# Optimization experiments

Measured on AMD Instinct MI355X. Metric: run time of the kernel, lower is better.

## Reference

```python
import jax, jax.numpy as jnp
import numpy as np

EPS = 1e-5


def conv2d(x, w, b, groups=1):
    # x: NCHW, w: OIHW, stride 1, SAME padding (== padding=k//2 for odd k)
    y = jax.lax.conv_general_dilated(
        x, w, window_strides=(1, 1), padding='SAME',
        dimension_numbers=('NCHW', 'OIHW', 'NCHW'),
        feature_group_count=groups)
    return y + b[None, :, None, None]


def gelu(x):
    return jax.nn.gelu(x, approximate=False)  # torch default GELU is exact erf


def adaptive_feature_norm(x, gamma, beta, s1w, s1b, s2w, s2b):
    # stats_net: GAP -> 1x1 conv -> ReLU -> 1x1 conv -> chunk into (gamma_a, beta_a)
    pooled = x.mean(axis=(2, 3), keepdims=True)                 # [B,C,1,1]
    h = jax.nn.relu(conv2d(pooled, s1w, s1b))
    stats = conv2d(h, s2w, s2b)                                 # [B,2C,1,1]
    ag, ab = jnp.split(stats, 2, axis=1)
    mean = x.mean(axis=(2, 3), keepdims=True)
    n = x.shape[2] * x.shape[3]
    var = ((x - mean) ** 2).sum(axis=(2, 3), keepdims=True) / (n - 1)  # unbiased, torch.var_mean default
    x_norm = (x - mean) * jax.lax.rsqrt(var + EPS)
    return (1 + ag) * gamma * x_norm + ab * beta


def setup_inputs() -> dict:
    key = jax.random.key(0)
    ks = jax.random.split(key, 40)
    B, C, H, W = 16, 256, 96, 96
    c4 = C // 4

    def n(k, shape, s=0.02):
        return jax.random.normal(k, shape, dtype=jnp.float32) * s

    inp = dict(
        x=jax.random.normal(ks[0], (B, C, H, W), dtype=jnp.float32),
        # branch1 conv1: dim -> dim//4, 3x3
        b1_conv1_w=n(ks[1], (c4, C, 3, 3)), b1_conv1_b=jnp.zeros((c4,), jnp.float32),
        # AFN on dim//4
        afn1_gamma=jnp.ones((1, c4, 1, 1), jnp.float32), afn1_beta=jnp.zeros((1, c4, 1, 1), jnp.float32),
        afn1_s1_w=n(ks[2], (c4 // 4, c4, 1, 1)), afn1_s1_b=jnp.zeros((c4 // 4,), jnp.float32),
        afn1_s2_w=n(ks[3], (c4 * 2, c4 // 4, 1, 1)), afn1_s2_b=jnp.zeros((c4 * 2,), jnp.float32),
        # branch1 conv2: dim//4 -> dim, 3x3
        b1_conv2_w=n(ks[4], (C, c4, 3, 3)), b1_conv2_b=jnp.zeros((C,), jnp.float32),
        # AFN on dim
        afn2_gamma=jnp.ones((1, C, 1, 1), jnp.float32), afn2_beta=jnp.zeros((1, C, 1, 1), jnp.float32),
        afn2_s1_w=n(ks[5], (c4, C, 1, 1)), afn2_s1_b=jnp.zeros((c4,), jnp.float32),
        afn2_s2_w=n(ks[6], (C * 2, c4, 1, 1)), afn2_s2_b=jnp.zeros((C * 2,), jnp.float32),
        # attention qkv/proj (1x1 convs)
        qkv_w=n(ks[7], (3 * C, C, 1, 1)), qkv_b=jnp.zeros((3 * C,), jnp.float32),
        proj_w=n(ks[8], (C, C, 1, 1)), proj_b=jnp.zeros((C,), jnp.float32),
        # 3 frequency decomposition branches, stacked
        # grouped 3x3 conv: groups=C//4, in=C (4 per group), out=C//4 (1 per group) -> weight [C//4, 4, 3, 3]
        fd_dw_w=n(ks[9], (3, c4, 4, 3, 3)), fd_dw_b=jnp.zeros((3, c4), jnp.float32),
        fd_pw_w=n(ks[10], (3, C, c4, 1, 1)), fd_pw_b=jnp.zeros((3, C), jnp.float32),
        freq_weights=jnp.ones((3,), jnp.float32),
        # router: GAP -> 1x1 conv -> softmax over 2 routes
        router_w=n(ks[11], (2, C, 1, 1)), router_b=jnp.zeros((2,), jnp.float32),
    )
    return inp


def reference(x,
              b1_conv1_w, b1_conv1_b, afn1_gamma, afn1_beta, afn1_s1_w, afn1_s1_b, afn1_s2_w, afn1_s2_b,
              b1_conv2_w, b1_conv2_b, afn2_gamma, afn2_beta, afn2_s1_w, afn2_s1_b, afn2_s2_w, afn2_s2_b,
              qkv_w, qkv_b, proj_w, proj_b, fd_dw_w, fd_dw_b, fd_pw_w, fd_pw_b, freq_weights,
              router_w, router_b):
    B, C, H, W = x.shape
    num_heads = 8
    hd = C // num_heads
    scale = C ** (-0.5)

    # ---- router ----
    pooled = x.mean(axis=(2, 3), keepdims=True)
    route = jax.nn.softmax(conv2d(pooled, router_w, router_b), axis=1)  # [B,2,1,1]

    # ---- branch1: conv -> AFN -> GELU -> conv -> AFN ----
    h = conv2d(x, b1_conv1_w, b1_conv1_b)
    h = adaptive_feature_norm(h, afn1_gamma, afn1_beta, afn1_s1_w, afn1_s1_b, afn1_s2_w, afn1_s2_b)
    h = gelu(h)
    h = conv2d(h, b1_conv2_w, b1_conv2_b)
    out1 = adaptive_feature_norm(h, afn2_gamma, afn2_beta, afn2_s1_w, afn2_s1_b, afn2_s2_w, afn2_s2_b)

    # ---- branch2: multi-scale frequency attention ----
    qkv = conv2d(x, qkv_w, qkv_b).reshape(B, 3, num_heads, hd, H, W)
    q, k, v = qkv[:, 0], qkv[:, 1], qkv[:, 2]          # [B, nh, hd, H, W]
    # attn over spatial rows: q @ k^T contracts W -> [B, nh, hd, H, H]
    attn = jnp.einsum('bndhw,bndgw->bndhg', q, k) * scale
    attn = jax.nn.softmax(attn, axis=-1)
    a = jnp.einsum('bndhg,bndgw->bndhw', attn, v)       # [B, nh, hd, H, W]
    # torch: .transpose(1, 2).reshape(B, C, H, W)  (hd-major channel order)
    a = a.transpose(0, 2, 1, 3, 4).reshape(B, C, H, W)
    x_attn = conv2d(a, proj_w, proj_b)

    fw = jax.nn.softmax(freq_weights, axis=0)
    freq_out = 0.0
    for i in range(3):
        f = conv2d(x, fd_dw_w[i], fd_dw_b[i], groups=C // 4)
        f = conv2d(gelu(f), fd_pw_w[i], fd_pw_b[i])
        freq_out = freq_out + fw[i] * f
    out2 = x_attn + freq_out

    return x + route[:, 0:1, :, :] * out1 + route[:, 1:2, :, :] * out2
```

## Files before the change

### kernel.cpp

```cpp
#include <hip/hip_runtime.h>
#include <hip/hip_bf16.h>
#include <math.h>
#include <stdint.h>

#define BB 16
#define CC 256
#define C4 64
#define HH 96
#define WW 96
#define HW 9216
#define EPSF 1e-5f

using bf16x8 = __attribute__((ext_vector_type(8))) short;
using bf16x4 = __attribute__((ext_vector_type(4))) short;
using f32x4  = __attribute__((ext_vector_type(4))) float;

#define GLD16(g, l) \
    __builtin_amdgcn_global_load_lds((const __attribute__((address_space(1))) unsigned int*)(g), \
                                     (__attribute__((address_space(3))) unsigned int*)(l), 16, 0, 0)

__device__ inline float bf2f_bits(short s) {
    return __uint_as_float(((unsigned int)(unsigned short)s) << 16);
}
__device__ inline short f2bf_bits(float f) {
    unsigned int u = __float_as_uint(f);
    return (short)((u + 0x7fffu + ((u >> 16) & 1u)) >> 16);
}

__global__ void zero_n_kernel(unsigned int* __restrict__ p, int n) {
    int i = blockIdx.x * 256 + threadIdx.x;
    if (i < n) p[i] = 0u;
}

__global__ void router_kernel(const float* __restrict__ pooled, const float* __restrict__ rw,
                              const float* __restrict__ rb, const float* __restrict__ fwts,
                              float* __restrict__ route, float* __restrict__ fw) {
    int t = threadIdx.x;
    const float invhw = 1.f / (float)HW;
    if (t < BB) {
        float l0 = rb[0], l1 = rb[1];
        for (int c = 0; c < CC; ++c) {
            float p = pooled[t * CC + c] * invhw;
            l0 += p * rw[c];
            l1 += p * rw[CC + c];
        }
        float m = fmaxf(l0, l1);
        float e0 = __expf(l0 - m), e1 = __expf(l1 - m);
        float inv = 1.f / (e0 + e1);
        route[t * 2 + 0] = e0 * inv;
        route[t * 2 + 1] = e1 * inv;
    }
    if (t == BB) {
        float a = fwts[0], b = fwts[1], c = fwts[2];
        float m = fmaxf(a, fmaxf(b, c));
        float e0 = __expf(a - m), e1 = __expf(b - m), e2 = __expf(c - m);
        float inv = 1.f / (e0 + e1 + e2);
        fw[0] = e0 * inv; fw[1] = e1 * inv; fw[2] = e2 * inv;
    }
}

__global__ void pack_w3x3_kernel(const float* __restrict__ w, __hip_bfloat16* __restrict__ wt,
                                 int COUT, int CINW) {
    int idx = blockIdx.x * 256 + threadIdx.x;
    int total = COUT * 9 * CINW;
    if (idx >= total) return;
    int ci = idx % CINW; int rest = idx / CINW; int tau = rest % 9; int co = rest / 9;
    wt[idx] = __float2bfloat16(w[((size_t)co * CINW + ci) * 9 + tau]);
}

__global__ void cast_w_kernel(const float* __restrict__ w, __hip_bfloat16* __restrict__ o, int n) {
    int idx = blockIdx.x * 256 + threadIdx.x;
    if (idx < n) o[idx] = __float2bfloat16(w[idx]);
}

__global__ void cast_w448_kernel(const float* __restrict__ w, __hip_bfloat16* __restrict__ A448) {
    int idx = blockIdx.x * 256 + threadIdx.x;
    int co = idx >> 8, ci = idx & 255;
    A448[co * 448 + ci] = __float2bfloat16(w[idx]);
}

__global__ void fuse_freq_w448_kernel(const float* __restrict__ pww, const float* __restrict__ pwb,
                                      const float* __restrict__ pjb, const float* __restrict__ fw,
                                      __hip_bfloat16* __restrict__ A448, float* __restrict__ fb448) {
    int co = blockIdx.x; int t = threadIdx.x;
    int i = t >> 6, g = t & 63;
    A448[co * 448 + 256 + t] = __float2bfloat16(fw[i] * pww[((size_t)(i * 256 + co)) * 64 + g]);
    if (t == 0) fb448[co] = pjb[co] + fw[0] * pwb[co] + fw[1] * pwb[256 + co] + fw[2] * pwb[512 + co];
}

__device__ inline float to_f32(float v) { return v; }
__device__ inline float to_f32(__hip_bfloat16 v) { return __bfloat162float(v); }

template <typename TIN, int CIN, int OSTR, bool POOL, bool AFN, bool GELU>
__global__ __launch_bounds__(256) void transpose_pm_kernel(const TIN* __restrict__ x,
                                                           __hip_bfloat16* __restrict__ xt,
                                                           float* __restrict__ pooled,
                                                           const float* __restrict__ mean,
                                                           const float* __restrict__ istd,
                                                           const float* __restrict__ ag,
                                                           const float* __restrict__ ab,
                                                           const float* __restrict__ gamma,
                                                           const float* __restrict__ beta) {
    __shared__ float s[32][33];
    __shared__ float ps[8][32];
    int p0 = blockIdx.x * 32, c0 = blockIdx.y * 32, b = blockIdx.z;
    int tx = threadIdx.x, ty = threadIdx.y;
    const TIN* xp = x + ((size_t)b * CIN + c0) * HW + p0;
#pragma unroll
    for (int i = 0; i < 4; ++i) {
        int c = ty * 4 + i;
        float v = to_f32(xp[(size_t)c * HW + tx]);
        if (AFN) {
            int bc = b * CIN + c0 + c;
            float sc = (1.f + ag[bc]) * gamma[c0 + c] * istd[bc];
            float sh = ab[bc] * beta[c0 + c];
            v = (v - mean[bc]) * sc + sh;
            if (GELU) v = 0.5f * v * (1.f + erff(v * 0.70710678118654752f));
        }
        s[c][tx] = v;
    }
    __syncthreads();
    __hip_bfloat16* yp = xt + ((size_t)b * HW + p0) * OSTR + c0;
#pragma unroll
    for (int i = 0; i < 4; ++i) {
        int r = ty * 4 + i;
        yp[(size_t)r * OSTR + tx] = __float2bfloat16(s[tx][r]);
    }
    if (POOL) {
        float l4 = 0.f;
#pragma unroll
        for (int i = 0; i < 4; ++i) l4 += s[tx][ty * 4 + i];
        ps[ty][tx] = l4;
        __syncthreads();
        if (ty == 0) {
            float tot = 0.f;
#pragma unroll
            for (int k = 0; k < 8; ++k) tot += ps[k][tx];
            atomicAdd(&pooled[b * CIN + c0 + tx], tot);
        }
    }
}

template <int BM, int BN, int TSH, int KC, int CDIM, int EPI, int CO_TOT, bool STATS>
__global__ __launch_bounds__(256) void mfma_gemm_kernel(const short* __restrict__ A,
                                                        const short* __restrict__ Bx,
                                                        const short* __restrict__ zp,
                                                        const float* __restrict__ bias,
                                                        const float* __restrict__ route,
                                                        void* __restrict__ Y,
                                                        float* __restrict__ ssum,
                                                        float* __restrict__ sssq,
                                                        int bin0, int bout0) {
    constexpr int WM = BM / 2, WN = BN / 2;
    constexpr int FM = WM / 16, FN = WN / 16;
    constexpr int KBT = KC / 64;
    constexpr int NS = TSH * KBT;
    constexpr int NA = BM / 16;
    constexpr int NB = BN / 16;
    __shared__ __align__(16) short As[2][2][BM * 32];
    __shared__ __align__(16) short Bs[2][2][BN * 32];
    int tid = threadIdx.x;
    int wid = tid >> 6, lane = tid & 63;
    int wy = wid >> 1, wx = wid & 1;
    int lane16 = lane & 15, quad = lane >> 4;
    int lrow = lane >> 2, lchk = lane & 3;
    int swz = (lrow >> 1) & 3;
    int co0 = blockIdx.x * BM;
    int n0 = blockIdx.y * BN;
    int bin = blockIdx.z + bin0;
    int bout = blockIdx.z + bout0;

    f32x4 acc[FM][FN];
#pragma unroll
    for (int i = 0; i < FM; ++i)
#pragma unroll
        for (int j = 0; j < FN; ++j) acc[i][j] = (f32x4){0.f, 0.f, 0.f, 0.f};

    const short* Bbase = Bx + (size_t)bin * HW * CDIM;

    auto stage = [&](int s, int d) {
        int tau = (TSH > 1) ? (s / KBT) : 0;
        int kb  = s - tau * KBT;
        int kc0 = kb * 64;
        int dh = tau / 3, dw = tau % 3;
        int off = (dh - 1) * 96 + (dw - 1);
        int ksw = kc0 + (lchk ^ swz) * 8;
#pragma unroll
        for (int kk = 0; kk < 2; ++kk) {
#pragma unroll
            for (int t = 0; t < NA / 4; ++t) {
                int inst = wid * (NA / 4) + t;
                int row = inst * 16 + lrow;
                const short* g = A + (size_t)(co0 + row) * (TSH * KC) + tau * KC + ksw + kk * 32;
                GLD16(g, &As[d][kk][inst * 512]);
            }
#pragma unroll
            for (int t = 0; t < NB / 4; ++t) {
                int inst = wid * (NB / 4) + t;
                int row = inst * 16 + lrow;
                int n = n0 + row;
                const short* g;
                if (TSH > 1) {
                    int h = n / 96, w = n - h * 96;
                    int hh = h + dh - 1, ww2 = w + dw - 1;
                    bool valid = ((unsigned)hh < 96u) && ((unsigned)ww2 < 96u);
                    g = valid ? (Bbase + (size_t)(n + off) * CDIM + ksw + kk * 32) : zp;
                } else {
                    g = Bbase + (size_t)n * CDIM + ksw + kk * 32;
                }
                GLD16(g, &Bs[d][kk][inst * 512]);
            }
        }
    };

    stage(0, 0);
    __syncthreads();
    for (int s = 0; s < NS; ++s) {
        int cur = s & 1;
        if (s + 1 < NS) stage(s + 1, cur ^ 1);
#pragma unroll
        for (int kk = 0; kk < 2; ++kk) {
            bf16x8 af[FM], bfr[FN];
#pragma unroll
            for (int i = 0; i < FM; ++i) {
                int row = wy * WM + i * 16 + lane16;
                int ch = (quad ^ ((row >> 1) & 3)) * 8;
                af[i] = *(const bf16x8*)&As[cur][kk][row * 32 + ch];
            }
#pragma unroll
            for (int j = 0; j < FN; ++j) {
                int row = wx * WN + j * 16 + lane16;
                int ch = (quad ^ ((row >> 1) & 3)) * 8;
                bfr[j] = *(const bf16x8*)&Bs[cur][kk][row * 32 + ch];
            }
#pragma unroll
            for (int i = 0; i < FM; ++i)
#pragma unroll
                for (int j = 0; j < FN; ++j)
                    acc[i][j] = __builtin_amdgcn_mfma_f32_16x16x32_bf16(af[i], bfr[j], acc[i][j], 0, 0, 0);
        }
        __syncthreads();
    }

    float scale = 1.f;
    if (EPI == 2) scale = route[bin * 2 + 1];
    float sl[FM][4], ql[FM][4];
    if (STATS) {
#pragma unroll
        for (int i = 0; i < FM; ++i)
#pragma unroll
            for (int r = 0; r < 4; ++r) { sl[i][r] = 0.f; ql[i][r] = 0.f; }
    }
#pragma unroll
    for (int i = 0; i < FM; ++i) {
        int co_l = co0 + wy * WM + i * 16 + quad * 4;
#pragma unroll
        for (int j = 0; j < FN; ++j) {
            int pix = n0 + wx * WN + j * 16 + lane16;
#pragma unroll
            for (int r = 0; r < 4; ++r) {
                int co = co_l + r;
                float v = acc[i][j][r] + bias[co];
                size_t idx = ((size_t)(bout * CO_TOT + co)) * HW + pix;
                if (EPI == 0) ((float*)Y)[idx] = v;
                else if (EPI == 1) ((__hip_bfloat16*)Y)[idx] = __float2bfloat16(v);
                else ((float*)Y)[idx] += scale * v;
                if (STATS) { sl[i][r] += v; ql[i][r] += v * v; }
            }
        }
    }
    if (STATS) {
#pragma unroll
        for (int i = 0; i < FM; ++i) {
            int co_l = co0 + wy * WM + i * 16 + quad * 4;
#pragma unroll
            for (int r = 0; r < 4; ++r) {
                float s = sl[i][r], q = ql[i][r];
                s += __shfl_xor(s, 1); q += __shfl_xor(q, 1);
                s += __shfl_xor(s, 2); q += __shfl_xor(q, 2);
                s += __shfl_xor(s, 4); q += __shfl_xor(q, 4);
                s += __shfl_xor(s, 8); q += __shfl_xor(q, 8);
                if (lane16 == 0) {
                    int bc = bout * CO_TOT + co_l + r;
                    atomicAdd(&ssum[bc], s);
                    atomicAdd(&sssq[bc], q);
                }
            }
        }
    }
}

__global__ void afn_finalize_kernel(const float* __restrict__ s, const float* __restrict__ q,
                                    float* __restrict__ mean, float* __restrict__ istd, int n) {
    int i = blockIdx.x * 256 + threadIdx.x;
    if (i >= n) return;
    float m = s[i] / (float)HW;
    float var = (q[i] - s[i] * m) / (float)(HW - 1);
    mean[i] = m;
    istd[i] = rsqrtf(var + EPSF);
}

template <int CH, int HID>
__global__ void afn_mlp_kernel(const float* __restrict__ mean,
                               const float* __restrict__ s1w, const float* __restrict__ s1b,
                               const float* __restrict__ s2w, const float* __restrict__ s2b,
                               float* __restrict__ ag, float* __restrict__ ab) {
    int b = blockIdx.x;
    __shared__ float hbuf[HID];
    int t = threadIdx.x;
    if (t < HID) {
        float s = s1b[t];
        for (int c = 0; c < CH; ++c) s += mean[b * CH + c] * s1w[t * CH + c];
        hbuf[t] = fmaxf(s, 0.f);
    }
    __syncthreads();
    if (t < 2 * CH) {
        float s = s2b[t];
#pragma unroll
        for (int k = 0; k < HID; ++k) s += hbuf[k] * s2w[t * HID + k];
        if (t < CH) ag[b * CH + t] = s;
        else        ab[b * CH + (t - CH)] = s;
    }
}

__global__ __launch_bounds__(256) void afn_combine_kernel(const float* __restrict__ x,
                                                          const float* __restrict__ h2,
                                                          const float* __restrict__ mean,
                                                          const float* __restrict__ istd,
                                                          const float* __restrict__ ag,
                                                          const float* __restrict__ ab,
                                                          const float* __restrict__ gamma,
                                                          const float* __restrict__ beta,
                                                          const float* __restrict__ route,
                                                          float* __restrict__ out) {
    int p4 = blockIdx.x * 256 + threadIdx.x;
    int c = blockIdx.y, b = blockIdx.z;
    int bc = b * CC + c;
    float scale = (1.f + ag[bc]) * gamma[c] * istd[bc];
    float shift = ab[bc] * beta[c];
    float m = mean[bc];
    float r0 = route[b * 2];
    size_t base = (size_t)bc * (HW / 4) + p4;
    const f32x4 xv = ((const f32x4*)x)[base];
    const f32x4 hv = ((const f32x4*)h2)[base];
    f32x4 o;
#pragma unroll
    for (int e = 0; e < 4; ++e) o[e] = xv[e] + r0 * ((hv[e] - m) * scale + shift);
    ((f32x4*)out)[base] = o;
}

__global__ __launch_bounds__(256) void vtrans_kernel(const __hip_bfloat16* __restrict__ qkv,
                                                     __hip_bfloat16* __restrict__ vt) {
    __shared__ __hip_bfloat16 s[32][34];
    int th = blockIdx.x / 3, tw = blockIdx.x % 3;
    int c = blockIdx.y, b = blockIdx.z;
    int tx = threadIdx.x, ty = threadIdx.y;
    const __hip_bfloat16* ip = qkv + ((size_t)b * 768 + 512 + c) * HW + (size_t)(th * 32) * 96 + tw * 32;
#pragma unroll
    for (int i = 0; i < 4; ++i) s[ty * 4 + i][tx] = ip[(size_t)(ty * 4 + i) * 96 + tx];
    __syncthreads();
    __hip_bfloat16* op = vt + ((size_t)b * 256 + c) * HW + (size_t)(tw * 32) * 96 + th * 32;
#pragma unroll
    for (int i = 0; i < 4; ++i) op[(size_t)(ty * 4 + i) * 96 + tx] = s[tx][ty * 4 + i];
}

__global__ __launch_bounds__(256) void attn_mfma_kernel(const __hip_bfloat16* __restrict__ qkv,
                                                        const __hip_bfloat16* __restrict__ vt,
                                                        __hip_bfloat16* __restrict__ a, int bout0) {
    int d = blockIdx.x, n = blockIdx.y, b = blockIdx.z;
    __shared__ __align__(16) __hip_bfloat16 Ps[96 * 104];
    int t = threadIdx.x;
    int lane = t & 63, wid = t >> 6;
    int wy = wid >> 1, wx = wid & 1;
    int lane16 = lane & 15, quad = lane >> 4;

    const __hip_bfloat16* qp = qkv + ((size_t)b * 768 + n * 32 + d) * HW;
    const __hip_bfloat16* kp = qp + (size_t)256 * HW;
    const __hip_bfloat16* vp = vt + ((size_t)b * 256 + n * 32 + d) * HW;

    f32x4 acc[3][3];
#pragma unroll
    for (int i = 0; i < 3; ++i)
#pragma unroll
        for (int j = 0; j < 3; ++j) acc[i][j] = (f32x4){0.f, 0.f, 0.f, 0.f};

#pragma unroll
    for (int kb = 0; kb < 3; ++kb) {
        int kc = kb * 32 + quad * 8;
        bf16x8 af[3], bfr[3];
#pragma unroll
        for (int i = 0; i < 3; ++i)
            af[i] = *(const bf16x8*)(qp + (size_t)(wy * 48 + i * 16 + lane16) * 96 + kc);
#pragma unroll
        for (int j = 0; j < 3; ++j)
            bfr[j] = *(const bf16x8*)(kp + (size_t)(wx * 48 + j * 16 + lane16) * 96 + kc);
#pragma unroll
        for (int i = 0; i < 3; ++i)
#pragma unroll
            for (int j = 0; j < 3; ++j)
                acc[i][j] = __builtin_amdgcn_mfma_f32_16x16x32_bf16(af[i], bfr[j], acc[i][j], 0, 0, 0);
    }

    const float scale = 0.0625f;
#pragma unroll
    for (int i = 0; i < 3; ++i) {
        int rbase = wy * 48 + i * 16 + quad * 4;
#pragma unroll
        for (int j = 0; j < 3; ++j) {
            int col = wx * 48 + j * 16 + lane16;
#pragma unroll
            for (int r = 0; r < 4; ++r)
                Ps[(rbase + r) * 104 + col] = __float2bfloat16(acc[i][j][r] * scale);
        }
    }
    __syncthreads();

    if (t < 192) {
        int row = t >> 1, hh = t & 1;
        const bf16x4* pr4 = (const bf16x4*)&Ps[row * 104 + hh * 48];
        float vb[48];
        float m = -1e30f;
#pragma unroll
        for (int j4 = 0; j4 < 12; ++j4) {
            bf16x4 u = pr4[j4];
#pragma unroll
            for (int e = 0; e < 4; ++e) {
                float f = bf2f_bits(u[e]);
                vb[j4 * 4 + e] = f;
                m = fmaxf(m, f);
            }
        }
        m = fmaxf(m, __shfl_xor(m, 1));
        float ssum = 0.f;
#pragma unroll
        for (int j2 = 0; j2 < 48; ++j2) { vb[j2] = __expf(vb[j2] - m); ssum += vb[j2]; }
        ssum += __shfl_xor(ssum, 1);
        float inv = 1.f / ssum;
        bf16x4* pw4 = (bf16x4*)&Ps[row * 104 + hh * 48];
#pragma unroll
        for (int j4 = 0; j4 < 12; ++j4) {
            bf16x4 o;
#pragma unroll
            for (int e = 0; e < 4; ++e) o[e] = f2bf_bits(vb[j4 * 4 + e] * inv);
            pw4[j4] = o;
        }
    }
    __syncthreads();

#pragma unroll
    for (int i = 0; i < 3; ++i)
#pragma unroll
        for (int j = 0; j < 3; ++j) acc[i][j] = (f32x4){0.f, 0.f, 0.f, 0.f};

#pragma unroll
    for (int kb = 0; kb < 3; ++kb) {
        int kc = kb * 32 + quad * 8;
        bf16x8 af[3], bfr[3];
#pragma unroll
        for (int i = 0; i < 3; ++i)
            af[i] = *(const bf16x8*)&Ps[(wy * 48 + i * 16 + lane16) * 104 + kc];
#pragma unroll
        for (int j = 0; j < 3; ++j)
            bfr[j] = *(const bf16x8*)(vp + (size_t)(wx * 48 + j * 16 + lane16) * 96 + kc);
#pragma unroll
        for (int i = 0; i < 3; ++i)
#pragma unroll
            for (int j = 0; j < 3; ++j)
                acc[i][j] = __builtin_amdgcn_mfma_f32_16x16x32_bf16(af[i], bfr[j], acc[i][j], 0, 0, 0);
    }

    __hip_bfloat16* ap = a + ((size_t)(bout0 + b) * CC + (d * 8 + n)) * HW;
#pragma unroll
    for (int i = 0; i < 3; ++i) {
        int rbase = wy * 48 + i * 16 + quad * 4;
#pragma unroll
        for (int j = 0; j < 3; ++j) {
            int col = wx * 48 + j * 16 + lane16;
#pragma unroll
            for (int r = 0; r < 4; ++r)
                ap[(size_t)(rbase + r) * 96 + col] = __float2bfloat16(acc[i][j][r]);
        }
    }
}

__global__ __launch_bounds__(256) void freq3_kernel(const float* __restrict__ x,
                                                    const float* __restrict__ dww,
                                                    const float* __restrict__ dwb,
                                                    __hip_bfloat16* __restrict__ f) {
    int p = blockIdx.x * 256 + threadIdx.x;
    int g = blockIdx.y;
    int b = blockIdx.z;
    int h = p / WW, w = p % WW;
    float a0 = dwb[g], a1 = dwb[64 + g], a2 = dwb[128 + g];
    const float* w0 = dww + g * 36;
    const float* w1 = dww + (64 + g) * 36;
    const float* w2 = dww + (128 + g) * 36;
#pragma unroll
    for (int q = 0; q < 4; ++q) {
        const float* xc = x + ((size_t)b * CC + 4 * g + q) * HW;
#pragma unroll
        for (int dh = 0; dh < 3; ++dh) {
            int hh = h + dh - 1;
            bool hv = (hh >= 0) && (hh < HH);
#pragma unroll
            for (int dw = 0; dw < 3; ++dw) {
                int ww2 = w + dw - 1;
                bool v = hv && (ww2 >= 0) && (ww2 < WW);
                float xv = v ? xc[hh * WW + ww2] : 0.f;
                int wi = q * 9 + dh * 3 + dw;
                a0 += xv * w0[wi];
                a1 += xv * w1[wi];
                a2 += xv * w2[wi];
            }
        }
    }
    a0 = 0.5f * a0 * (1.f + erff(a0 * 0.70710678118654752f));
    a1 = 0.5f * a1 * (1.f + erff(a1 * 0.70710678118654752f));
    a2 = 0.5f * a2 * (1.f + erff(a2 * 0.70710678118654752f));
    size_t base = ((size_t)b * 192 + g) * HW + p;
    f[base] = __float2bfloat16(a0);
    f[base + (size_t)64 * HW] = __float2bfloat16(a1);
    f[base + (size_t)128 * HW] = __float2bfloat16(a2);
}

extern "C" void kernel_launch(void* const* d_in, const int* in_sizes, int n_in,
                              void* d_out, int out_size, void* d_ws, size_t ws_size,
                              hipStream_t stream) {
    const float* x    = (const float*)d_in[0];
    const float* c1w  = (const float*)d_in[1];
    const float* c1b  = (const float*)d_in[2];
    const float* g1   = (const float*)d_in[3];
    const float* be1  = (const float*)d_in[4];
    const float* s1w1 = (const float*)d_in[5];
    const float* s1b1 = (const float*)d_in[6];
    const float* s2w1 = (const float*)d_in[7];
    const float* s2b1 = (const float*)d_in[8];
    const float* c2w  = (const float*)d_in[9];
    const float* c2b  = (const float*)d_in[10];
    const float* g2   = (const float*)d_in[11];
    const float* be2  = (const float*)d_in[12];
    const float* s1w2 = (const float*)d_in[13];
    const float* s1b2 = (const float*)d_in[14];
    const float* s2w2 = (const float*)d_in[15];
    const float* s2b2 = (const float*)d_in[16];
    const float* qkvw = (const float*)d_in[17];
    const float* qkvb = (const float*)d_in[18];
    const float* pjw  = (const float*)d_in[19];
    const float* pjb  = (const float*)d_in[20];
    const float* dww  = (const float*)d_in[21];
    const float* dwb  = (const float*)d_in[22];
    const float* pww  = (const float*)d_in[23];
    const float* pwb  = (const float*)d_in[24];
    const float* fwts = (const float*)d_in[25];
    const float* rw   = (const float*)d_in[26];
    const float* rb   = (const float*)d_in[27];
    float* out = (float*)d_out;
    (void)ws_size;

    char* ws = (char*)d_ws;
    float* h2 = (float*)ws;
    __hip_bfloat16* qkvs = (__hip_bfloat16*)ws;
    __hip_bfloat16* fall = (__hip_bfloat16*)ws;
    __hip_bfloat16* ftA = (__hip_bfloat16*)(ws + 56623104ULL);
    __hip_bfloat16* vt = (__hip_bfloat16*)(ws + 113246208ULL);
    float* h1 = (float*)(ws + 150994944ULL);
    __hip_bfloat16* h1t = (__hip_bfloat16*)(ws + 188743680ULL);
    __hip_bfloat16* xt = (__hip_bfloat16*)(ws + 207618048ULL);
    __hip_bfloat16* at = xt;
    const size_t TB = 283115520ULL;
    short* zp = (short*)(ws + TB);
    float* zf = (float*)(ws + TB + 256);
    float* ssum1  = zf;
    float* sssq1  = zf + 1024;
    float* ssum2  = zf + 2048;
    float* sssq2  = zf + 6144;
    float* pooled = zf + 10240;
    float* route  = zf + 14336;
    float* fw     = zf + 14368;
    float* mean1  = zf + 14372;
    float* istd1  = zf + 15396;
    float* ag1    = zf + 16420;
    float* ab1    = zf + 17444;
    float* mean2  = zf + 18468;
    float* istd2  = zf + 22564;
    float* ag2    = zf + 26660;
    float* ab2    = zf + 30756;
    float* fb448  = zf + 34852;
    char* wbase = (char*)(zf + 35108);
    __hip_bfloat16* wt1  = (__hip_bfloat16*)wbase;
    __hip_bfloat16* wt2  = (__hip_bfloat16*)(wbase + 294912);
    __hip_bfloat16* qw16 = (__hip_bfloat16*)(wbase + 589824);
    __hip_bfloat16* A448 = (__hip_bfloat16*)(wbase + 983040);

    zero_n_kernel<<<57, 256, 0, stream>>>((unsigned int*)zp, 14400);

    transpose_pm_kernel<float, 256, 256, true, false, false>
        <<<dim3(288, 8, 16), dim3(32, 8), 0, stream>>>(x, xt, pooled, nullptr, nullptr,
                                                       nullptr, nullptr, nullptr, nullptr);
    router_kernel<<<1, 64, 0, stream>>>(pooled, rw, rb, fwts, route, fw);

    pack_w3x3_kernel<<<576, 256, 0, stream>>>(c1w, wt1, 64, 256);
    pack_w3x3_kernel<<<576, 256, 0, stream>>>(c2w, wt2, 256, 64);
    cast_w_kernel<<<768, 256, 0, stream>>>(qkvw, qw16, 768 * 256);
    cast_w448_kernel<<<256, 256, 0, stream>>>(pjw, A448);
    fuse_freq_w448_kernel<<<256, 192, 0, stream>>>(pww, pwb, pjb, fw, A448, fb448);

    mfma_gemm_kernel<64, 128, 9, 256, 256, 0, 64, true>
        <<<dim3(1, 72, 16), 256, 0, stream>>>((const short*)wt1, (const short*)xt, zp, c1b,
                                              nullptr, h1, ssum1, sssq1, 0, 0);
    afn_finalize_kernel<<<4, 256, 0, stream>>>(ssum1, sssq1, mean1, istd1, BB * C4);
    afn_mlp_kernel<64, 16><<<dim3(BB), 128, 0, stream>>>(mean1, s1w1, s1b1, s2w1, s2b1, ag1, ab1);
    transpose_pm_kernel<float, 64, 64, false, true, true>
        <<<dim3(288, 2, 16), dim3(32, 8), 0, stream>>>(h1, h1t, nullptr, mean1, istd1,
                                                       ag1, ab1, g1, be1);
    mfma_gemm_kernel<128, 128, 9, 64, 64, 0, 256, true>
        <<<dim3(2, 72, 16), 256, 0, stream>>>((const short*)wt2, (const short*)h1t, zp, c2b,
                                              nullptr, h2, ssum2, sssq2, 0, 0);
    afn_finalize_kernel<<<16, 256, 0, stream>>>(ssum2, sssq2, mean2, istd2, BB * CC);
    afn_mlp_kernel<256, 64><<<dim3(BB), 512, 0, stream>>>(mean2, s1w2, s1b2, s2w2, s2b2, ag2, ab2);
    afn_combine_kernel<<<dim3(9, 256, 16), 256, 0, stream>>>(x, h2, mean2, istd2, ag2, ab2,
                                                             g2, be2, route, out);

    for (int half = 0; half < 2; ++half) {
        mfma_gemm_kernel<128, 128, 1, 256, 256, 1, 768, false>
            <<<dim3(6, 72, 8), 256, 0, stream>>>((const short*)qw16, (const short*)xt, zp, qkvb,
                                                 nullptr, qkvs, nullptr, nullptr, half * 8, 0);
        vtrans_kernel<<<dim3(9, 256, 8), dim3(32, 8), 0, stream>>>(qkvs, vt);
        attn_mfma_kernel<<<dim3(32, 8, 8), 256, 0, stream>>>(qkvs, vt, at, half * 8);
    }

    freq3_kernel<<<dim3(36, 64, 16), 256, 0, stream>>>(x, dww, dwb, fall);

    transpose_pm_kernel<__hip_bfloat16, 256, 448, false, false, false>
        <<<dim3(288, 8, 16), dim3(32, 8), 0, stream>>>(at, ftA, nullptr, nullptr, nullptr,
                                                       nullptr, nullptr, nullptr, nullptr);
    transpose_pm_kernel<__hip_bfloat16, 192, 448, false, false, false>
        <<<dim3(288, 6, 16), dim3(32, 8), 0, stream>>>(fall, ftA + 256, nullptr, nullptr, nullptr,
                                                       nullptr, nullptr, nullptr, nullptr);

    mfma_gemm_kernel<128, 128, 1, 448, 448, 2, 256, false>
        <<<dim3(2, 72, 16), 256, 0, stream>>>((const short*)A448, (const short*)ftA, zp, fb448,
                                              route, out, nullptr, nullptr, 0, 0);
}
```

Measured before the change: 1.224 ms.

## Add dedicated 3x3 conv kernel reusing a shared halo tile across horizontal taps

Adds a dedicated 3x3 convolution kernel. For each vertical tap and K chunk it stages one 160-row slab of input pixels (the 128-pixel tile plus a halo) into LDS, then reads all three horizontal taps from that slab at shifted row offsets. Row-edge pixels are zeroed with per-lane masks. Previously all nine taps were staged separately from global memory. Weights are now read straight from global into registers instead of through LDS, and the generic GEMM loses its im2col and stats paths. This cuts global traffic for the input by about 3x, at the cost of uncached weight loads per tap and a 64-row output tile for the second conv.

```diff
diff --git a/kernel.cpp b/kernel.cpp
--- a/kernel.cpp
+++ b/kernel.cpp
@@ -141,20 +141,155 @@
     }
 }
 
-template <int BM, int BN, int TSH, int KC, int CDIM, int EPI, int CO_TOT, bool STATS>
+template <int KC, int CDIM, int CO_TOT>
+__global__ __launch_bounds__(256) void conv3x3_kernel(const short* __restrict__ A,
+                                                      const short* __restrict__ Bx,
+                                                      const short* __restrict__ zp,
+                                                      const float* __restrict__ bias,
+                                                      float* __restrict__ Y,
+                                                      float* __restrict__ ssum,
+                                                      float* __restrict__ sssq) {
+    constexpr int BM = 64, BN = 128, WN = 64;
+    constexpr int FM = 2, FN = 4;
+    constexpr int KBC = KC / 64;
+    constexpr int NS = 3 * KBC;
+    constexpr int SROWS = 160;
+    __shared__ __align__(16) short Bs[2][SROWS * 64];
+    int tid = threadIdx.x;
+    int wid = tid >> 6, lane = tid & 63;
+    int wy = wid >> 1, wx = wid & 1;
+    int lane16 = lane & 15, quad = lane >> 4;
+    int co0 = blockIdx.x * BM;
+    int n0 = blockIdx.y * BN;
+    int b = blockIdx.z;
+    const short* Bbase = Bx + (size_t)b * HW * CDIM;
+
+    bool m0[FN], m2[FN];
+#pragma unroll
+    for (int j = 0; j < FN; ++j) {
+        int n = n0 + wx * WN + j * 16 + lane16;
+        int w = n % 96;
+        m0[j] = (w == 0);
+        m2[j] = (w == 95);
+    }
+
+    int srow_l = lane >> 3;
+    int schunk = (lane & 7) ^ srow_l;
+
+    auto stage = [&](int s, int d) {
+        int dh = s / KBC, kb = s - dh * KBC;
+        int kc0 = kb * 64;
+        int mb = n0 - 16 + (dh - 1) * 96;
+#pragma unroll
+        for (int t = 0; t < 5; ++t) {
+            int inst = wid * 5 + t;
+            int m = mb + inst * 8 + srow_l;
+            const short* g = ((unsigned)m < (unsigned)HW)
+                                 ? (Bbase + (size_t)m * CDIM + kc0 + schunk * 8)
+                                 : zp;
+            GLD16(g, &Bs[d][inst * 512]);
+        }
+    };
+
+    f32x4 acc[FM][FN];
+#pragma unroll
+    for (int i = 0; i < FM; ++i)
+#pragma unroll
+        for (int j = 0; j < FN; ++j) acc[i][j] = (f32x4){0.f, 0.f, 0.f, 0.f};
+
+    const bf16x8 Z8 = (bf16x8){0, 0, 0, 0, 0, 0, 0, 0};
+
+    stage(0, 0);
+    __syncthreads();
+    for (int s = 0; s < NS; ++s) {
+        int cur = s & 1;
+        if (s + 1 < NS) stage(s + 1, cur ^ 1);
+        int dh = s / KBC, kb = s - dh * KBC;
+        int kc0 = kb * 64;
+#pragma unroll
+        for (int dw = 0; dw < 3; ++dw) {
+            int tau = dh * 3 + dw;
+            bf16x8 af[2][FM];
+#pragma unroll
+            for (int kk = 0; kk < 2; ++kk)
+#pragma unroll
+                for (int i = 0; i < FM; ++i)
+                    af[kk][i] = *(const bf16x8*)(A + (size_t)(co0 + wy * 32 + i * 16 + lane16) * (9 * KC)
+                                                 + tau * KC + kc0 + kk * 32 + quad * 8);
+            bf16x8 bfr[2][FN];
+#pragma unroll
+            for (int kk = 0; kk < 2; ++kk)
+#pragma unroll
+                for (int j = 0; j < FN; ++j) {
+                    int srow = wx * WN + j * 16 + lane16 + 15 + dw;
+                    int cs = (quad + 4 * kk) ^ (srow & 7);
+                    bf16x8 v = *(const bf16x8*)&Bs[cur][srow * 64 + cs * 8];
+                    if (dw == 0) { if (m0[j]) v = Z8; }
+                    else if (dw == 2) { if (m2[j]) v = Z8; }
+                    bfr[kk][j] = v;
+                }
+#pragma unroll
+            for (int kk = 0; kk < 2; ++kk)
+#pragma unroll
+                for (int i = 0; i < FM; ++i)
+#pragma unroll
+                    for (int j = 0; j < FN; ++j)
+                        acc[i][j] = __builtin_amdgcn_mfma_f32_16x16x32_bf16(af[kk][i], bfr[kk][j],
+                                                                            acc[i][j], 0, 0, 0);
+        }
+        __syncthreads();
+    }
+
+    float sl[FM][4], ql[FM][4];
+#pragma unroll
+    for (int i = 0; i < FM; ++i)
+#pragma unroll
+        for (int r = 0; r < 4; ++r) { sl[i][r] = 0.f; ql[i][r] = 0.f; }
+#pragma unroll
+    for (int i = 0; i < FM; ++i) {
+        int co_l = co0 + wy * 32 + i * 16 + quad * 4;
+#pragma unroll
+        for (int j = 0; j < FN; ++j) {
+            int pix = n0 + wx * WN + j * 16 + lane16;
+#pragma unroll
+            for (int r = 0; r < 4; ++r) {
+                int co = co_l + r;
+                float v = acc[i][j][r] + bias[co];
+                Y[((size_t)(b * CO_TOT + co)) * HW + pix] = v;
+                sl[i][r] += v; ql[i][r] += v * v;
+            }
+        }
+    }
+#pragma unroll
+    for (int i = 0; i < FM; ++i) {
+        int co_l = co0 + wy * 32 + i * 16 + quad * 4;
+#pragma unroll
+        for (int r = 0; r < 4; ++r) {
+            float s = sl[i][r], q = ql[i][r];
+            s += __shfl_xor(s, 1); q += __shfl_xor(q, 1);
+            s += __shfl_xor(s, 2); q += __shfl_xor(q, 2);
+            s += __shfl_xor(s, 4); q += __shfl_xor(q, 4);
+            s += __shfl_xor(s, 8); q += __shfl_xor(q, 8);
+            if (lane16 == 0) {
+                int bc = b * CO_TOT + co_l + r;
+                atomicAdd(&ssum[bc], s);
+                atomicAdd(&sssq[bc], q);
+            }
+        }
+    }
+}
+
+template <int BM, int BN, int KC, int CDIM, int EPI, int CO_TOT>
 __global__ __launch_bounds__(256) void mfma_gemm_kernel(const short* __restrict__ A,
                                                         const short* __restrict__ Bx,
                                                         const short* __restrict__ zp,
                                                         const float* __restrict__ bias,
                                                         const float* __restrict__ route,
                                                         void* __restrict__ Y,
-                                                        float* __restrict__ ssum,
-                                                        float* __restrict__ sssq,
                                                         int bin0, int bout0) {
     constexpr int WM = BM / 2, WN = BN / 2;
     constexpr int FM = WM / 16, FN = WN / 16;
-    constexpr int KBT = KC / 64;
-    constexpr int NS = TSH * KBT;
+    constexpr int NS = KC / 64;
     constexpr int NA = BM / 16;
     constexpr int NB = BN / 16;
     __shared__ __align__(16) short As[2][2][BM * 32];
@@ -179,11 +314,7 @@
     const short* Bbase = Bx + (size_t)bin * HW * CDIM;
 
     auto stage = [&](int s, int d) {
-        int tau = (TSH > 1) ? (s / KBT) : 0;
-        int kb  = s - tau * KBT;
-        int kc0 = kb * 64;
-        int dh = tau / 3, dw = tau % 3;
-        int off = (dh - 1) * 96 + (dw - 1);
+        int kc0 = s * 64;
         int ksw = kc0 + (lchk ^ swz) * 8;
 #pragma unroll
         for (int kk = 0; kk < 2; ++kk) {
@@ -191,23 +322,14 @@
             for (int t = 0; t < NA / 4; ++t) {
                 int inst = wid * (NA / 4) + t;
                 int row = inst * 16 + lrow;
-                const short* g = A + (size_t)(co0 + row) * (TSH * KC) + tau * KC + ksw + kk * 32;
+                const short* g = A + (size_t)(co0 + row) * KC + ksw + kk * 32;
                 GLD16(g, &As[d][kk][inst * 512]);
             }
 #pragma unroll
             for (int t = 0; t < NB / 4; ++t) {
                 int inst = wid * (NB / 4) + t;
                 int row = inst * 16 + lrow;
-                int n = n0 + row;
-                const short* g;
-                if (TSH > 1) {
-                    int h = n / 96, w = n - h * 96;
-                    int hh = h + dh - 1, ww2 = w + dw - 1;
-                    bool valid = ((unsigned)hh < 96u) && ((unsigned)ww2 < 96u);
-                    g = valid ? (Bbase + (size_t)(n + off) * CDIM + ksw + kk * 32) : zp;
-                } else {
-                    g = Bbase + (size_t)n * CDIM + ksw + kk * 32;
-                }
+                const short* g = Bbase + (size_t)(n0 + row) * CDIM + ksw + kk * 32;
                 GLD16(g, &Bs[d][kk][inst * 512]);
             }
         }
@@ -244,13 +366,6 @@
 
     float scale = 1.f;
     if (EPI == 2) scale = route[bin * 2 + 1];
-    float sl[FM][4], ql[FM][4];
-    if (STATS) {
-#pragma unroll
-        for (int i = 0; i < FM; ++i)
-#pragma unroll
-            for (int r = 0; r < 4; ++r) { sl[i][r] = 0.f; ql[i][r] = 0.f; }
-    }
 #pragma unroll
     for (int i = 0; i < FM; ++i) {
         int co_l = co0 + wy * WM + i * 16 + quad * 4;
@@ -262,29 +377,8 @@
                 int co = co_l + r;
                 float v = acc[i][j][r] + bias[co];
                 size_t idx = ((size_t)(bout * CO_TOT + co)) * HW + pix;
-                if (EPI == 0) ((float*)Y)[idx] = v;
-                else if (EPI == 1) ((__hip_bfloat16*)Y)[idx] = __float2bfloat16(v);
+                if (EPI == 1) ((__hip_bfloat16*)Y)[idx] = __float2bfloat16(v);
                 else ((float*)Y)[idx] += scale * v;
-                if (STATS) { sl[i][r] += v; ql[i][r] += v * v; }
-            }
-        }
-    }
-    if (STATS) {
-#pragma unroll
-        for (int i = 0; i < FM; ++i) {
-            int co_l = co0 + wy * WM + i * 16 + quad * 4;
-#pragma unroll
-            for (int r = 0; r < 4; ++r) {
-                float s = sl[i][r], q = ql[i][r];
-                s += __shfl_xor(s, 1); q += __shfl_xor(q, 1);
-                s += __shfl_xor(s, 2); q += __shfl_xor(q, 2);
-                s += __shfl_xor(s, 4); q += __shfl_xor(q, 4);
-                s += __shfl_xor(s, 8); q += __shfl_xor(q, 8);
-                if (lane16 == 0) {
-                    int bc = bout * CO_TOT + co_l + r;
-                    atomicAdd(&ssum[bc], s);
-                    atomicAdd(&sssq[bc], q);
-                }
             }
         }
     }
@@ -605,26 +699,26 @@
     cast_w448_kernel<<<256, 256, 0, stream>>>(pjw, A448);
     fuse_freq_w448_kernel<<<256, 192, 0, stream>>>(pww, pwb, pjb, fw, A448, fb448);
 
-    mfma_gemm_kernel<64, 128, 9, 256, 256, 0, 64, true>
+    conv3x3_kernel<256, 256, 64>
         <<<dim3(1, 72, 16), 256, 0, stream>>>((const short*)wt1, (const short*)xt, zp, c1b,
-                                              nullptr, h1, ssum1, sssq1, 0, 0);
+                                              h1, ssum1, sssq1);
     afn_finalize_kernel<<<4, 256, 0, stream>>>(ssum1, sssq1, mean1, istd1, BB * C4);
     afn_mlp_kernel<64, 16><<<dim3(BB), 128, 0, stream>>>(mean1, s1w1, s1b1, s2w1, s2b1, ag1, ab1);
     transpose_pm_kernel<float, 64, 64, false, true, true>
         <<<dim3(288, 2, 16), dim3(32, 8), 0, stream>>>(h1, h1t, nullptr, mean1, istd1,
                                                        ag1, ab1, g1, be1);
-    mfma_gemm_kernel<128, 128, 9, 64, 64, 0, 256, true>
-        <<<dim3(2, 72, 16), 256, 0, stream>>>((const short*)wt2, (const short*)h1t, zp, c2b,
-                                              nullptr, h2, ssum2, sssq2, 0, 0);
+    conv3x3_kernel<64, 64, 256>
+        <<<dim3(4, 72, 16), 256, 0, stream>>>((const short*)wt2, (const short*)h1t, zp, c2b,
+                                              h2, ssum2, sssq2);
     afn_finalize_kernel<<<16, 256, 0, stream>>>(ssum2, sssq2, mean2, istd2, BB * CC);
     afn_mlp_kernel<256, 64><<<dim3(BB), 512, 0, stream>>>(mean2, s1w2, s1b2, s2w2, s2b2, ag2, ab2);
     afn_combine_kernel<<<dim3(9, 256, 16), 256, 0, stream>>>(x, h2, mean2, istd2, ag2, ab2,
                                                              g2, be2, route, out);
 
     for (int half = 0; half < 2; ++half) {
-        mfma_gemm_kernel<128, 128, 1, 256, 256, 1, 768, false>
+        mfma_gemm_kernel<128, 128, 256, 256, 1, 768>
             <<<dim3(6, 72, 8), 256, 0, stream>>>((const short*)qw16, (const short*)xt, zp, qkvb,
-                                                 nullptr, qkvs, nullptr, nullptr, half * 8, 0);
+                                                 nullptr, qkvs, half * 8, 0);
         vtrans_kernel<<<dim3(9, 256, 8), dim3(32, 8), 0, stream>>>(qkvs, vt);
         attn_mfma_kernel<<<dim3(32, 8, 8), 256, 0, stream>>>(qkvs, vt, at, half * 8);
     }
@@ -638,7 +732,7 @@
         <<<dim3(288, 6, 16), dim3(32, 8), 0, stream>>>(fall, ftA + 256, nullptr, nullptr, nullptr,
                                                        nullptr, nullptr, nullptr, nullptr);
 
-    mfma_gemm_kernel<128, 128, 1, 448, 448, 2, 256, false>
+    mfma_gemm_kernel<128, 128, 448, 448, 2, 256>
         <<<dim3(2, 72, 16), 256, 0, stream>>>((const short*)A448, (const short*)ftA, zp, fb448,
-                                              route, out, nullptr, nullptr, 0, 0);
-}
+                                              route, out, 0, 0);
+}
```

After: 1.239 ms. No clear change (+1.2%).
